# Performance work log

Measured on AMD Instinct MI355X. Metric: run time of the kernel, lower is better.

The kernel has to match this reference:

```python
import jax, jax.numpy as jnp
import numpy as np

NEG_SLOPE = 0.01  # torch F.leaky_relu default


def _safediv(a, b):
    b = jnp.where(b == 0, jnp.ones_like(b), b)
    return a / b


def setup_inputs() -> dict:
    key = jax.random.key(0)
    ks = jax.random.split(key, 5)
    N, K, IN, HID, OUT = 50000, 32, 128, 128, 128
    h_node = jax.random.normal(ks[0], (N, IN), dtype=jnp.float32)
    h_ngbrs = jax.random.normal(ks[1], (N, K, IN), dtype=jnp.float32)
    alpha = jax.random.uniform(ks[2], (N, K, 1), dtype=jnp.float32)
    # xavier_uniform with relu gain, biases zero (as in the torch init)
    gain = float(np.sqrt(2.0))
    lim_q = gain * np.sqrt(6.0 / (IN + HID))
    lim_w = gain * np.sqrt(6.0 / (IN + HID + OUT))
    Wq = jax.random.uniform(ks[3], (HID, IN), dtype=jnp.float32, minval=-lim_q, maxval=lim_q)
    Ww = jax.random.uniform(ks[4], (OUT, IN + HID), dtype=jnp.float32, minval=-lim_w, maxval=lim_w)
    bq = jnp.zeros((HID,), dtype=jnp.float32)
    bw = jnp.zeros((OUT,), dtype=jnp.float32)
    return {"h_node": h_node, "h_ngbrs": h_ngbrs, "alpha": alpha,
            "Wq": Wq, "bq": bq, "Ww": Ww, "bw": bw}


def reference(h_node, h_ngbrs, alpha, Wq, bq, Ww, bw):
    # h_ngbrs: [N, K, IN] -> LeakyReLU(Q(h_ngbrs)): [N, K, HID]
    h1 = jax.nn.leaky_relu(jnp.einsum('nki,hi->nkh', h_ngbrs, Wq) + bq, NEG_SLOPE)
    # weighted mean over neighbors: alpha [N, K, 1]
    h_agg = _safediv((alpha * h1).sum(axis=1), alpha.sum(axis=1))  # [N, HID]
    h_concat = jnp.concatenate([h_node, h_agg], axis=-1)           # [N, IN+HID]
    h2 = jax.nn.leaky_relu(h_concat @ Ww.T + bw, NEG_SLOPE)        # [N, OUT]
    nrm = jnp.linalg.norm(h2, axis=-1, keepdims=True)              # per-node L2 norm
    return _safediv(h2, nrm)
```

## Files before the change

kernel.cpp:

```cpp
#include <hip/hip_runtime.h>

#define NNODES 50000
#define DIN 128
#define DHID 128
#define DOUT 128
#define NEG_SLOPE 0.01f
#define NT 12500
#define GG 256

typedef _Float16 f16x8 __attribute__((ext_vector_type(8)));
typedef _Float16 f16x4 __attribute__((ext_vector_type(4)));
typedef _Float16 f16x2 __attribute__((ext_vector_type(2)));
typedef float f32x4 __attribute__((ext_vector_type(4)));

__device__ __forceinline__ f16x2 pkrtz(float a, float b) {
    return __builtin_bit_cast(f16x2, __builtin_amdgcn_cvt_pkrtz(a, b));
}

#define WS_WQ_HI 0
#define WS_WQ_LO 16384
#define WS_WW_HI 32768
#define WS_WW_LO 65536

__device__ __forceinline__ void gload_lds16(const float* g, float* lds) {
    __builtin_amdgcn_global_load_lds(
        (const __attribute__((address_space(1))) void*)g,
        (__attribute__((address_space(3))) void*)lds, 16, 0, 0);
}

__global__ void convert_weights(const float* __restrict__ Wq,
                                const float* __restrict__ Ww,
                                _Float16* __restrict__ ws) {
    int id = blockIdx.x * 256 + threadIdx.x;
    if (id < 2048) {
        int s  = id;
        int l  = s & 63;
        int g  = (s >> 6) & 3;
        int ct = s >> 8;
        int col = ct * 16 + (l & 15);
        int k0  = g * 32 + (l >> 4) * 8;
        const float* src = Wq + col * DIN + k0;
        f16x8 vh, vl;
#pragma unroll
        for (int j = 0; j < 8; ++j) {
            float v = src[j];
            _Float16 h = (_Float16)v;
            vh[j] = h;
            vl[j] = (_Float16)(v - (float)h);
        }
        *(f16x8*)(ws + WS_WQ_HI + s * 8) = vh;
        *(f16x8*)(ws + WS_WQ_LO + s * 8) = vl;
    } else if (id < 2048 + 4096) {
        int s  = id - 2048;
        int l  = s & 63;
        int g  = (s >> 6) & 7;
        int ct = s >> 9;
        int col = ct * 16 + (l & 15);
        int k0  = g * 32 + (l >> 4) * 8;
        const float* src = Ww + col * (DIN + DHID) + k0;
        f16x8 vh, vl;
#pragma unroll
        for (int j = 0; j < 8; ++j) {
            float v = src[j];
            _Float16 h = (_Float16)v;
            vh[j] = h;
            vl[j] = (_Float16)(v - (float)h);
        }
        *(f16x8*)(ws + WS_WW_HI + s * 8) = vh;
        *(f16x8*)(ws + WS_WW_LO + s * 8) = vl;
    }
}

__global__ __launch_bounds__(512, 2) void gemm1_agg(
    const float* __restrict__ hng,
    const float* __restrict__ alpha,
    const float* __restrict__ bq,
    const _Float16* __restrict__ ws,
    float* __restrict__ hagg)
{
    __shared__ float As[2][16384];

    const int tid = threadIdx.x;
    const int l   = tid & 63;
    const int wid = tid >> 6;
    const int wr  = wid >> 2;
    const int wc  = wid & 3;
    const int r16 = l & 15;
    const int kg  = l >> 4;

    const _Float16* wqh = ws + WS_WQ_HI;
    const _Float16* wql = ws + WS_WQ_LO;

    f16x8 bh[4][2], bl[4][2];
#pragma unroll
    for (int kf = 0; kf < 4; ++kf)
#pragma unroll
        for (int ct = 0; ct < 2; ++ct) {
            int off = (((wc * 2 + ct) * 4 + kf) * 64 + l) * 8;
            bh[kf][ct] = *(const f16x8*)(wqh + off);
            bl[kf][ct] = *(const f16x8*)(wql + off);
        }

    int so[8];
#pragma unroll
    for (int i = 0; i < 8; ++i) {
        int row = (wid * 8 + i) * 2 + (l >> 5);
        int o   = (l & 31) * 16;
        so[i]   = row * 128 + ((o ^ ((row & 7) << 4)) >> 2);
    }

    float bqv[2];
#pragma unroll
    for (int ct = 0; ct < 2; ++ct)
        bqv[ct] = bq[wc * 32 + ct * 16 + r16];

#define STAGE(Rb, s)                                                          \
    do {                                                                      \
        _Pragma("unroll")                                                     \
        for (int i_ = 0; i_ < 8; ++i_) {                                      \
            gload_lds16(hng + (long)(Rb)*DIN + so[i_],                        \
                        &As[s][(wid * 8 + i_) * 256]);                        \
        }                                                                     \
    } while (0)

#define COMPUTE(s)                                                            \
    do {                                                                      \
        _Pragma("unroll")                                                     \
        for (int rt_ = 0; rt_ < 4; ++rt_) {                                   \
            int row_ = wr * 64 + rt_ * 16 + r16;                              \
            int asw_ = (row_ & 7) << 4;                                       \
            const char* sb_ = (const char*)&As[s][0] + row_ * 512;            \
            _Pragma("unroll")                                                 \
            for (int kf_ = 0; kf_ < 4; ++kf_) {                               \
                int kb_ = kf_ * 128 + kg * 32;                                \
                f32x4 v0_ = *(const f32x4*)(sb_ + ((kb_ + 0) ^ asw_));        \
                f32x4 v1_ = *(const f32x4*)(sb_ + ((kb_ + 16) ^ asw_));       \
                f16x2 p0_ = pkrtz(v0_[0], v0_[1]);                            \
                f16x2 p1_ = pkrtz(v0_[2], v0_[3]);                            \
                f16x2 p2_ = pkrtz(v1_[0], v1_[1]);                            \
                f16x2 p3_ = pkrtz(v1_[2], v1_[3]);                            \
                f16x8 ah_;                                                    \
                ah_[0] = p0_[0]; ah_[1] = p0_[1];                             \
                ah_[2] = p1_[0]; ah_[3] = p1_[1];                             \
                ah_[4] = p2_[0]; ah_[5] = p2_[1];                             \
                ah_[6] = p3_[0]; ah_[7] = p3_[1];                             \
                _Pragma("unroll")                                             \
                for (int ct_ = 0; ct_ < 2; ++ct_) {                           \
                    acc[rt_][ct_] = __builtin_amdgcn_mfma_f32_16x16x32_f16(   \
                        ah_, bh[kf_][ct_], acc[rt_][ct_], 0, 0, 0);           \
                    acc[rt_][ct_] = __builtin_amdgcn_mfma_f32_16x16x32_f16(   \
                        ah_, bl[kf_][ct_], acc[rt_][ct_], 0, 0, 0);           \
                }                                                             \
            }                                                                 \
        }                                                                     \
    } while (0)

    long t  = blockIdx.x;
    long R0 = t * 128;

    STAGE(R0, 0);
    f32x4 av4[4];
#pragma unroll
    for (int rt = 0; rt < 4; ++rt)
        av4[rt] = *(const f32x4*)(alpha + R0 + wr * 64 + rt * 16 + kg * 4);
    asm volatile("s_waitcnt vmcnt(0)" ::: "memory");
    __builtin_amdgcn_s_barrier();
    __builtin_amdgcn_sched_barrier(0);

    int cur = 0;
    for (;;) {
        const bool last = (t + GG >= NT);
        const long tn   = last ? t : t + GG;
        const long Rn   = tn * 128;

        f32x4 acc[4][2];
#pragma unroll
        for (int i = 0; i < 4; ++i)
#pragma unroll
            for (int j = 0; j < 2; ++j) acc[i][j] = (f32x4){0.f, 0.f, 0.f, 0.f};

        asm volatile("s_waitcnt vmcnt(6)" ::: "memory");
        __builtin_amdgcn_s_barrier();
        __builtin_amdgcn_sched_barrier(0);
        STAGE(Rn, cur ^ 1);
        __builtin_amdgcn_sched_barrier(0);
        COMPUTE(cur);
        __builtin_amdgcn_sched_barrier(0);

        {
            float part[2][2] = {{0.f, 0.f}, {0.f, 0.f}};
            float apart[2] = {0.f, 0.f};
#pragma unroll
            for (int rt = 0; rt < 4; ++rt) {
                const int nl = rt >> 1;
#pragma unroll
                for (int r = 0; r < 4; ++r) {
                    float aw = av4[rt][r];
                    apart[nl] += aw;
#pragma unroll
                    for (int ct = 0; ct < 2; ++ct) {
                        float v = acc[rt][ct][r] + bqv[ct];
                        v = (v >= 0.f) ? v : NEG_SLOPE * v;
                        part[nl][ct] += aw * v;
                    }
                }
            }
#pragma unroll
            for (int nl = 0; nl < 2; ++nl) {
                apart[nl] += __shfl_xor(apart[nl], 16);
                apart[nl] += __shfl_xor(apart[nl], 32);
#pragma unroll
                for (int ct = 0; ct < 2; ++ct) {
                    part[nl][ct] += __shfl_xor(part[nl][ct], 16);
                    part[nl][ct] += __shfl_xor(part[nl][ct], 32);
                }
            }
            if (kg < 2) {
                int nl = kg;
                long node = t * 4 + wr * 2 + nl;
                float den = apart[nl];
                if (den == 0.f) den = 1.f;
#pragma unroll
                for (int ct = 0; ct < 2; ++ct) {
                    int col = wc * 32 + ct * 16 + r16;
                    hagg[node * DHID + col] = part[nl][ct] / den;
                }
            }
        }
        __builtin_amdgcn_sched_barrier(0);
#pragma unroll
        for (int rt = 0; rt < 4; ++rt)
            av4[rt] = *(const f32x4*)(alpha + Rn + wr * 64 + rt * 16 + kg * 4);
        __builtin_amdgcn_sched_barrier(0);

        if (last) break;
        t   = tn;
        R0  = Rn;
        cur ^= 1;
    }
    asm volatile("s_waitcnt vmcnt(0)" ::: "memory");

#undef STAGE
#undef COMPUTE
}

__global__ __launch_bounds__(256, 2) void gemm2_norm(
    const float* __restrict__ hnode,
    const float* __restrict__ bw,
    const _Float16* __restrict__ ws,
    float* __restrict__ out)
{
    __shared__ _Float16 Ahi[8 * 520];
    __shared__ _Float16 Bhi[8 * 512];
    __shared__ _Float16 Blo[8 * 512];
    __shared__ float bw_s[128];
    __shared__ float nbuf[2][128];

    const int tid = threadIdx.x;
    const int l   = tid & 63;
    const int wid = tid >> 6;
    const int wr  = wid >> 1, wc = wid & 1;
    const long NB = (long)blockIdx.x * 128;

    if (tid < 128) bw_s[tid] = bw[tid];

    f32x4 acc[4][4];
#pragma unroll
    for (int i = 0; i < 4; ++i)
#pragma unroll
        for (int j = 0; j < 4; ++j) acc[i][j] = (f32x4){0.f, 0.f, 0.f, 0.f};

    const _Float16* wwh = ws + WS_WW_HI;
    const _Float16* wwl = ws + WS_WW_LO;

    for (int c = 0; c < 8; ++c) {
        __syncthreads();
#pragma unroll
        for (int p = 0; p < 4; ++p) {
            int rl = p * 32 + (tid >> 3);
            long n = NB + rl;
            if (n > NNODES - 1) n = NNODES - 1;
            int kw = (tid & 7) * 4;
            int kgl = c * 32 + kw;
            const float* g = (kgl < 128) ? (hnode + n * DIN + kgl)
                                         : (out + n * DHID + (kgl - 128));
            f32x4 v = *(const f32x4*)g;
            f16x2 p0 = pkrtz(v[0], v[1]);
            f16x2 p1 = pkrtz(v[2], v[3]);
            f16x4 vh;
            vh[0] = p0[0]; vh[1] = p0[1]; vh[2] = p1[0]; vh[3] = p1[1];
            int lw  = (rl & 15) | (((kw >> 3) & 3) << 4);
            int s   = rl >> 4;
            int off = s * 520 + lw * 8 + (kw & 7);
            *(f16x4*)(Ahi + off) = vh;
        }
#pragma unroll
        for (int i = 0; i < 4; ++i) {
            int id = i * 256 + tid;
            int sb = id >> 6;
            int ls = id & 63;
            if (sb < 8) {
                *(f16x8*)(Bhi + sb * 512 + ls * 8) =
                    *(const f16x8*)(wwh + ((sb * 8 + c) * 64 + ls) * 8);
            } else {
                int ct = sb - 8;
                *(f16x8*)(Blo + ct * 512 + ls * 8) =
                    *(const f16x8*)(wwl + ((ct * 8 + c) * 64 + ls) * 8);
            }
        }
        __syncthreads();
        f16x8 ah[4], bh[4], bl[4];
#pragma unroll
        for (int rt = 0; rt < 4; ++rt) {
            int s = wr * 4 + rt;
            ah[rt] = *(const f16x8*)(Ahi + s * 520 + l * 8);
        }
#pragma unroll
        for (int ct = 0; ct < 4; ++ct) {
            int s = wc * 4 + ct;
            bh[ct] = *(const f16x8*)(Bhi + s * 512 + l * 8);
            bl[ct] = *(const f16x8*)(Blo + s * 512 + l * 8);
        }
#pragma unroll
        for (int rt = 0; rt < 4; ++rt)
#pragma unroll
            for (int ct = 0; ct < 4; ++ct) {
                acc[rt][ct] = __builtin_amdgcn_mfma_f32_16x16x32_f16(ah[rt], bh[ct], acc[rt][ct], 0, 0, 0);
                acc[rt][ct] = __builtin_amdgcn_mfma_f32_16x16x32_f16(ah[rt], bl[ct], acc[rt][ct], 0, 0, 0);
            }
    }

    const int grp = l >> 4;
#pragma unroll
    for (int rt = 0; rt < 4; ++rt)
#pragma unroll
        for (int ct = 0; ct < 4; ++ct)
#pragma unroll
            for (int r = 0; r < 4; ++r) {
                int col = wc * 64 + ct * 16 + (l & 15);
                float v = acc[rt][ct][r] + bw_s[col];
                acc[rt][ct][r] = (v >= 0.f) ? v : NEG_SLOPE * v;
            }
    float ssq[4][4];
#pragma unroll
    for (int rt = 0; rt < 4; ++rt)
#pragma unroll
        for (int r = 0; r < 4; ++r) {
            float s = 0.f;
#pragma unroll
            for (int ct = 0; ct < 4; ++ct) s += acc[rt][ct][r] * acc[rt][ct][r];
            s += __shfl_xor(s, 1);
            s += __shfl_xor(s, 2);
            s += __shfl_xor(s, 4);
            s += __shfl_xor(s, 8);
            ssq[rt][r] = s;
        }
    if ((l & 15) == 0) {
#pragma unroll
        for (int rt = 0; rt < 4; ++rt)
#pragma unroll
            for (int r = 0; r < 4; ++r)
                nbuf[wc][wr * 64 + rt * 16 + grp * 4 + r] = ssq[rt][r];
    }
    __syncthreads();
#pragma unroll
    for (int rt = 0; rt < 4; ++rt)
#pragma unroll
        for (int r = 0; r < 4; ++r) {
            int rowl = wr * 64 + rt * 16 + grp * 4 + r;
            long n = NB + rowl;
            if (n < NNODES) {
                float nrm = sqrtf(nbuf[0][rowl] + nbuf[1][rowl]);
                if (nrm == 0.f) nrm = 1.f;
#pragma unroll
                for (int ct = 0; ct < 4; ++ct) {
                    int col = wc * 64 + ct * 16 + (l & 15);
                    out[n * DOUT + col] = acc[rt][ct][r] / nrm;
                }
            }
        }
}

extern "C" void kernel_launch(void* const* d_in, const int* in_sizes, int n_in,
                              void* d_out, int out_size, void* d_ws, size_t ws_size,
                              hipStream_t stream) {
    const float* h_node  = (const float*)d_in[0];
    const float* h_ngbrs = (const float*)d_in[1];
    const float* alpha   = (const float*)d_in[2];
    const float* Wq      = (const float*)d_in[3];
    const float* bq      = (const float*)d_in[4];
    const float* Ww      = (const float*)d_in[5];
    const float* bw      = (const float*)d_in[6];
    float* out   = (float*)d_out;
    _Float16* ws = (_Float16*)d_ws;

    convert_weights<<<24, 256, 0, stream>>>(Wq, Ww, ws);
    gemm1_agg<<<GG, 512, 0, stream>>>(h_ngbrs, alpha, bq, ws, out);
    gemm2_norm<<<391, 256, 0, stream>>>(h_node, bw, ws, out);
}
```

Before: 232.8 us.

## Deepen gemm1 pipeline to four 64-row stages with alpha staged via LDS

Halves the tile per iteration (64 rows, two nodes) and moves from double to quadruple buffering, so three tiles are in flight while one is computed. Alpha values are now loaded asynchronously into LDS alongside the activations instead of through separate register loads. The goal is to hide more HBM latency on this bandwidth-bound gemm. In exchange there are more loop iterations and barriers, and the outstanding-load wait counts have to be exactly right.

```diff
diff --git a/kernel.cpp b/kernel.cpp
--- a/kernel.cpp
+++ b/kernel.cpp
@@ -5,7 +5,7 @@
 #define DHID 128
 #define DOUT 128
 #define NEG_SLOPE 0.01f
-#define NT 12500
+#define NT 25000
 #define GG 256
 
 typedef _Float16 f16x8 __attribute__((ext_vector_type(8)));
@@ -26,6 +26,11 @@
     __builtin_amdgcn_global_load_lds(
         (const __attribute__((address_space(1))) void*)g,
         (__attribute__((address_space(3))) void*)lds, 16, 0, 0);
+}
+__device__ __forceinline__ void gload_lds4(const float* g, float* lds) {
+    __builtin_amdgcn_global_load_lds(
+        (const __attribute__((address_space(1))) void*)g,
+        (__attribute__((address_space(3))) void*)lds, 4, 0, 0);
 }
 
 __global__ void convert_weights(const float* __restrict__ Wq,
@@ -78,7 +83,8 @@
     const _Float16* __restrict__ ws,
     float* __restrict__ hagg)
 {
-    __shared__ float As[2][16384];
+    __shared__ float As[4][8192];
+    __shared__ float Alp[4][64];
 
     const int tid = threadIdx.x;
     const int l   = tid & 63;
@@ -101,10 +107,10 @@
             bl[kf][ct] = *(const f16x8*)(wql + off);
         }
 
-    int so[8];
-#pragma unroll
-    for (int i = 0; i < 8; ++i) {
-        int row = (wid * 8 + i) * 2 + (l >> 5);
+    int so[4];
+#pragma unroll
+    for (int i = 0; i < 4; ++i) {
+        int row = (wid * 4 + i) * 2 + (l >> 5);
         int o   = (l & 31) * 16;
         so[i]   = row * 128 + ((o ^ ((row & 7) << 4)) >> 2);
     }
@@ -114,20 +120,21 @@
     for (int ct = 0; ct < 2; ++ct)
         bqv[ct] = bq[wc * 32 + ct * 16 + r16];
 
-#define STAGE(Rb, s)                                                          \
+#define STAGE(Tb, s)                                                          \
     do {                                                                      \
+        const float* gb_ = hng + (long)(Tb) * 64 * DIN;                       \
+        float* lb_ = &As[s][0];                                               \
         _Pragma("unroll")                                                     \
-        for (int i_ = 0; i_ < 8; ++i_) {                                      \
-            gload_lds16(hng + (long)(Rb)*DIN + so[i_],                        \
-                        &As[s][(wid * 8 + i_) * 256]);                        \
-        }                                                                     \
+        for (int i_ = 0; i_ < 4; ++i_)                                        \
+            gload_lds16(gb_ + so[i_], lb_ + (wid * 4 + i_) * 256);            \
+        gload_lds4(alpha + (long)(Tb) * 64 + l, &Alp[s][0]);                  \
     } while (0)
 
 #define COMPUTE(s)                                                            \
     do {                                                                      \
         _Pragma("unroll")                                                     \
-        for (int rt_ = 0; rt_ < 4; ++rt_) {                                   \
-            int row_ = wr * 64 + rt_ * 16 + r16;                              \
+        for (int rt_ = 0; rt_ < 2; ++rt_) {                                   \
+            int row_ = wr * 32 + rt_ * 16 + r16;                              \
             int asw_ = (row_ & 7) << 4;                                       \
             const char* sb_ = (const char*)&As[s][0] + row_ * 512;            \
             _Pragma("unroll")                                                 \
@@ -155,14 +162,11 @@
         }                                                                     \
     } while (0)
 
-    long t  = blockIdx.x;
-    long R0 = t * 128;
-
-    STAGE(R0, 0);
-    f32x4 av4[4];
-#pragma unroll
-    for (int rt = 0; rt < 4; ++rt)
-        av4[rt] = *(const f32x4*)(alpha + R0 + wr * 64 + rt * 16 + kg * 4);
+    long t = blockIdx.x;
+
+    STAGE(t, 0);
+    STAGE(t + GG, 1);
+    STAGE(t + 2 * GG, 2);
     asm volatile("s_waitcnt vmcnt(0)" ::: "memory");
     __builtin_amdgcn_s_barrier();
     __builtin_amdgcn_sched_barrier(0);
@@ -170,73 +174,65 @@
     int cur = 0;
     for (;;) {
         const bool last = (t + GG >= NT);
-        const long tn   = last ? t : t + GG;
-        const long Rn   = tn * 128;
-
-        f32x4 acc[4][2];
-#pragma unroll
-        for (int i = 0; i < 4; ++i)
+        const long ts   = (t + 3L * GG < NT) ? (t + 3L * GG) : t;
+        const int sstg  = (cur + 3) & 3;
+
+        f32x4 acc[2][2];
+#pragma unroll
+        for (int i = 0; i < 2; ++i)
 #pragma unroll
             for (int j = 0; j < 2; ++j) acc[i][j] = (f32x4){0.f, 0.f, 0.f, 0.f};
 
-        asm volatile("s_waitcnt vmcnt(6)" ::: "memory");
+        asm volatile("s_waitcnt vmcnt(16)" ::: "memory");
         __builtin_amdgcn_s_barrier();
         __builtin_amdgcn_sched_barrier(0);
-        STAGE(Rn, cur ^ 1);
+        STAGE(ts, sstg);
         __builtin_amdgcn_sched_barrier(0);
         COMPUTE(cur);
         __builtin_amdgcn_sched_barrier(0);
 
         {
-            float part[2][2] = {{0.f, 0.f}, {0.f, 0.f}};
-            float apart[2] = {0.f, 0.f};
-#pragma unroll
-            for (int rt = 0; rt < 4; ++rt) {
-                const int nl = rt >> 1;
-#pragma unroll
-                for (int r = 0; r < 4; ++r) {
-                    float aw = av4[rt][r];
-                    apart[nl] += aw;
-#pragma unroll
-                    for (int ct = 0; ct < 2; ++ct) {
-                        float v = acc[rt][ct][r] + bqv[ct];
-                        v = (v >= 0.f) ? v : NEG_SLOPE * v;
-                        part[nl][ct] += aw * v;
-                    }
-                }
-            }
-#pragma unroll
-            for (int nl = 0; nl < 2; ++nl) {
-                apart[nl] += __shfl_xor(apart[nl], 16);
-                apart[nl] += __shfl_xor(apart[nl], 32);
-#pragma unroll
-                for (int ct = 0; ct < 2; ++ct) {
-                    part[nl][ct] += __shfl_xor(part[nl][ct], 16);
-                    part[nl][ct] += __shfl_xor(part[nl][ct], 32);
-                }
-            }
-            if (kg < 2) {
-                int nl = kg;
-                long node = t * 4 + wr * 2 + nl;
-                float den = apart[nl];
+            f32x4 aw0 = *(const f32x4*)&Alp[cur][wr * 32 + kg * 4];
+            f32x4 aw1 = *(const f32x4*)&Alp[cur][wr * 32 + 16 + kg * 4];
+            float part0 = 0.f, part1 = 0.f, apart = 0.f;
+#pragma unroll
+            for (int r = 0; r < 4; ++r) {
+                float aw = aw0[r];
+                apart += aw;
+                float v = acc[0][0][r] + bqv[0];
+                v = (v >= 0.f) ? v : NEG_SLOPE * v;
+                part0 += aw * v;
+                v = acc[0][1][r] + bqv[1];
+                v = (v >= 0.f) ? v : NEG_SLOPE * v;
+                part1 += aw * v;
+            }
+#pragma unroll
+            for (int r = 0; r < 4; ++r) {
+                float aw = aw1[r];
+                apart += aw;
+                float v = acc[1][0][r] + bqv[0];
+                v = (v >= 0.f) ? v : NEG_SLOPE * v;
+                part0 += aw * v;
+                v = acc[1][1][r] + bqv[1];
+                v = (v >= 0.f) ? v : NEG_SLOPE * v;
+                part1 += aw * v;
+            }
+            part0 += __shfl_xor(part0, 16); part0 += __shfl_xor(part0, 32);
+            part1 += __shfl_xor(part1, 16); part1 += __shfl_xor(part1, 32);
+            apart += __shfl_xor(apart, 16); apart += __shfl_xor(apart, 32);
+            if (l < 16) {
+                long node = t * 2 + wr;
+                float den = apart;
                 if (den == 0.f) den = 1.f;
-#pragma unroll
-                for (int ct = 0; ct < 2; ++ct) {
-                    int col = wc * 32 + ct * 16 + r16;
-                    hagg[node * DHID + col] = part[nl][ct] / den;
-                }
+                hagg[node * DHID + wc * 32 + r16]      = part0 / den;
+                hagg[node * DHID + wc * 32 + 16 + r16] = part1 / den;
             }
         }
         __builtin_amdgcn_sched_barrier(0);
-#pragma unroll
-        for (int rt = 0; rt < 4; ++rt)
-            av4[rt] = *(const f32x4*)(alpha + Rn + wr * 64 + rt * 16 + kg * 4);
-        __builtin_amdgcn_sched_barrier(0);
 
         if (last) break;
-        t   = tn;
-        R0  = Rn;
-        cur ^= 1;
+        t  += GG;
+        cur = (cur + 1) & 3;
     }
     asm volatile("s_waitcnt vmcnt(0)" ::: "memory");
 
```

Measured after the change: 263.9 us. 13.4% more time.

## Stage neighbor tiles through registers instead of direct global-to-LDS loads

Applied to the files above, without the earlier changes.

Replaces the async global_load_lds staging of the h_ngbrs tile with register prefetch: the next tile and its alpha weights are loaded into registers before compute, then written to swizzled LDS after the aggregation, followed by one barrier. This removes the vmcnt wait and barrier before each stage and lets global latency overlap with MFMA compute. In exchange it costs 32 extra VGPRs for the prefetched tile plus explicit ds_write traffic, which may hurt occupancy.

```diff
diff --git a/kernel.cpp b/kernel.cpp
--- a/kernel.cpp
+++ b/kernel.cpp
@@ -21,12 +21,6 @@
 #define WS_WQ_LO 16384
 #define WS_WW_HI 32768
 #define WS_WW_LO 65536
-
-__device__ __forceinline__ void gload_lds16(const float* g, float* lds) {
-    __builtin_amdgcn_global_load_lds(
-        (const __attribute__((address_space(1))) void*)g,
-        (__attribute__((address_space(3))) void*)lds, 16, 0, 0);
-}
 
 __global__ void convert_weights(const float* __restrict__ Wq,
                                 const float* __restrict__ Ww,
@@ -101,12 +95,13 @@
             bl[kf][ct] = *(const f16x8*)(wql + off);
         }
 
-    int so[8];
+    int gro[8], dwo[8];
 #pragma unroll
     for (int i = 0; i < 8; ++i) {
         int row = (wid * 8 + i) * 2 + (l >> 5);
         int o   = (l & 31) * 16;
-        so[i]   = row * 128 + ((o ^ ((row & 7) << 4)) >> 2);
+        gro[i]  = row * 128 + (l & 31) * 4;
+        dwo[i]  = row * 512 + (o ^ ((row & 7) << 4));
     }
 
     float bqv[2];
@@ -114,13 +109,26 @@
     for (int ct = 0; ct < 2; ++ct)
         bqv[ct] = bq[wc * 32 + ct * 16 + r16];
 
-#define STAGE(Rb, s)                                                          \
+    f32x4 sA[8];
+    f32x4 av4[4], av4n[4];
+
+#define LOADR(Rb)                                                             \
     do {                                                                      \
         _Pragma("unroll")                                                     \
-        for (int i_ = 0; i_ < 8; ++i_) {                                      \
-            gload_lds16(hng + (long)(Rb)*DIN + so[i_],                        \
-                        &As[s][(wid * 8 + i_) * 256]);                        \
-        }                                                                     \
+        for (int i_ = 0; i_ < 8; ++i_)                                        \
+            sA[i_] = *(const f32x4*)(hng + (long)(Rb)*DIN + gro[i_]);         \
+        _Pragma("unroll")                                                     \
+        for (int rt_ = 0; rt_ < 4; ++rt_)                                     \
+            av4n[rt_] = *(const f32x4*)(alpha + (Rb) + wr * 64 + rt_ * 16 +   \
+                                        kg * 4);                              \
+    } while (0)
+
+#define DSWRITE(s)                                                            \
+    do {                                                                      \
+        char* lb_ = (char*)&As[s][0];                                         \
+        _Pragma("unroll")                                                     \
+        for (int i_ = 0; i_ < 8; ++i_)                                        \
+            *(f32x4*)(lb_ + dwo[i_]) = sA[i_];                                \
     } while (0)
 
 #define COMPUTE(s)                                                            \
@@ -158,12 +166,11 @@
     long t  = blockIdx.x;
     long R0 = t * 128;
 
-    STAGE(R0, 0);
-    f32x4 av4[4];
-#pragma unroll
-    for (int rt = 0; rt < 4; ++rt)
-        av4[rt] = *(const f32x4*)(alpha + R0 + wr * 64 + rt * 16 + kg * 4);
-    asm volatile("s_waitcnt vmcnt(0)" ::: "memory");
+    LOADR(R0);
+    DSWRITE(0);
+#pragma unroll
+    for (int rt = 0; rt < 4; ++rt) av4[rt] = av4n[rt];
+    asm volatile("s_waitcnt lgkmcnt(0)" ::: "memory");
     __builtin_amdgcn_s_barrier();
     __builtin_amdgcn_sched_barrier(0);
 
@@ -173,17 +180,15 @@
         const long tn   = last ? t : t + GG;
         const long Rn   = tn * 128;
 
+        LOADR(Rn);
+        __builtin_amdgcn_sched_barrier(0);
+
         f32x4 acc[4][2];
 #pragma unroll
         for (int i = 0; i < 4; ++i)
 #pragma unroll
             for (int j = 0; j < 2; ++j) acc[i][j] = (f32x4){0.f, 0.f, 0.f, 0.f};
 
-        asm volatile("s_waitcnt vmcnt(6)" ::: "memory");
-        __builtin_amdgcn_s_barrier();
-        __builtin_amdgcn_sched_barrier(0);
-        STAGE(Rn, cur ^ 1);
-        __builtin_amdgcn_sched_barrier(0);
         COMPUTE(cur);
         __builtin_amdgcn_sched_barrier(0);
 
@@ -228,9 +233,12 @@
             }
         }
         __builtin_amdgcn_sched_barrier(0);
-#pragma unroll
-        for (int rt = 0; rt < 4; ++rt)
-            av4[rt] = *(const f32x4*)(alpha + Rn + wr * 64 + rt * 16 + kg * 4);
+
+        DSWRITE(cur ^ 1);
+#pragma unroll
+        for (int rt = 0; rt < 4; ++rt) av4[rt] = av4n[rt];
+        asm volatile("s_waitcnt lgkmcnt(0)" ::: "memory");
+        __builtin_amdgcn_s_barrier();
         __builtin_amdgcn_sched_barrier(0);
 
         if (last) break;
@@ -240,7 +248,8 @@
     }
     asm volatile("s_waitcnt vmcnt(0)" ::: "memory");
 
-#undef STAGE
+#undef LOADR
+#undef DSWRITE
 #undef COMPUTE
 }
 
```

Measured after the change: 235.6 us. No clear change (+1.2%).
